# Kernel optimization log

Measured on AMD Instinct MI355X. Metric: run time of the kernel, lower is better.

Reference implementation:

```python
import jax, jax.numpy as jnp
import numpy as np
from math import sqrt

B, L, S, H, E = 4, 2048, 2048, 16, 64


def setup_inputs() -> dict:
    key = jax.random.key(0)
    kq, kk, kv = jax.random.split(key, 3)
    queries = jax.random.normal(kq, (B, L, H, E), dtype=jnp.float32)
    keys = jax.random.normal(kk, (B, S, H, E), dtype=jnp.float32)
    values = jax.random.normal(kv, (B, S, H, E), dtype=jnp.float32)
    # causal mask: True where attention is disallowed (upper triangle, excl diag)
    causal = jnp.triu(jnp.ones((L, S), dtype=jnp.bool_), k=1)
    attention_mask = jnp.broadcast_to(causal[None, None, :, :], (B, 1, L, S))
    return {"queries": queries, "keys": keys, "values": values,
            "attention_mask": attention_mask}


def reference(queries, keys, values, attention_mask):
    E_ = queries.shape[-1]
    scale = 1.0 / sqrt(E_)
    # [B,H,L,S] full score matrix (the quadratic intermediate of naive attention)
    scores = jnp.einsum('blhe,bshe->bhls', queries, keys)
    scores = jnp.where(attention_mask, -jnp.inf, scores)
    A = jnp.nan_to_num(jax.nn.softmax(scale * scores, axis=-1))
    V = jnp.einsum('bhls,bshd->blhd', A, values)
    return V
```

## Files before the change

kernel.cpp:

```cpp
#include <hip/hip_runtime.h>
#include <cmath>

#define B_ 4
#define L_ 2048
#define S_ 2048
#define H_ 16
#define E_ 64
#define SCALE2 0.18033688011112042f

typedef __attribute__((ext_vector_type(4))) float f32x4;
typedef __attribute__((ext_vector_type(8))) __bf16 bf16x8;
typedef __attribute__((ext_vector_type(8))) unsigned short ushort8;
union FragU { ushort8 u; bf16x8 b; unsigned int d[4]; };

__device__ __forceinline__ unsigned short f2bf(float f) {
    unsigned int u = __float_as_uint(f);
    return (unsigned short)((u + 0x7FFFu + ((u >> 16) & 1u)) >> 16);
}

__device__ __forceinline__ unsigned int pack_bf(float hi, float lo) {
    return __builtin_amdgcn_perm(__float_as_uint(hi), __float_as_uint(lo),
                                 0x07060302u);
}

__device__ __forceinline__ void gload_lds16(const void* g, void* l) {
    __builtin_amdgcn_global_load_lds(
        (const __attribute__((address_space(1))) void*)g,
        (__attribute__((address_space(3))) void*)l, 16, 0, 0);
}

__global__ __launch_bounds__(256) void conv_k(const float* __restrict__ K,
                                              unsigned short* __restrict__ Kbf) {
    const int idx = blockIdx.x * 256 + threadIdx.x;
    const int j   = idx & 7;
    const int row = idx >> 3;
    const int s   = row & (S_ - 1);
    const int bh  = row >> 11;
    const int h   = bh & (H_ - 1);
    const int b   = bh >> 4;
    const int jp  = j ^ (s & 7);
    const float* src = K + (((size_t)b * S_ + s) * H_ + h) * E_ + jp * 8;
    f32x4 a = *(const f32x4*)src;
    f32x4 d = *(const f32x4*)(src + 4);
    ushort8 u;
    u[0]=f2bf(a[0]); u[1]=f2bf(a[1]); u[2]=f2bf(a[2]); u[3]=f2bf(a[3]);
    u[4]=f2bf(d[0]); u[5]=f2bf(d[1]); u[6]=f2bf(d[2]); u[7]=f2bf(d[3]);
    *(ushort8*)(Kbf + (size_t)row * E_ + j * 8) = u;
}

__global__ __launch_bounds__(256) void conv_v(const float* __restrict__ V,
                                              unsigned short* __restrict__ Vt) {
    __shared__ unsigned short t[64 * 65];
    const int tid  = threadIdx.x;
    const int sblk = blockIdx.x & 31;
    const int h    = (blockIdx.x >> 5) & 15;
    const int b    = blockIdx.x >> 9;
    const int s0   = sblk * 64;
    for (int i = 0; i < 4; ++i) {
        const int c = tid + i * 256;
        const int sr = c >> 4, e0 = (c & 15) * 4;
        f32x4 a = *(const f32x4*)(V + (((size_t)b * S_ + s0 + sr) * H_ + h) * E_ + e0);
        t[sr * 65 + e0 + 0] = f2bf(a[0]);
        t[sr * 65 + e0 + 1] = f2bf(a[1]);
        t[sr * 65 + e0 + 2] = f2bf(a[2]);
        t[sr * 65 + e0 + 3] = f2bf(a[3]);
    }
    __syncthreads();
    for (int i = 0; i < 2; ++i) {
        const int c  = tid + i * 256;
        const int e  = c >> 3, cc = c & 7;
        const int q  = cc >> 1, half = cc & 1;
        ushort8 u;
        for (int j = 0; j < 8; ++j) {
            const int d = j >> 2, r = j & 3;
            const int key = (2 * half + d) * 16 + q * 4 + r;
            u[j] = t[key * 65 + e];
        }
        *(ushort8*)(Vt + ((size_t)(b * H_ + h) * E_ + e) * S_ + s0
                    + (cc ^ (e & 7)) * 8) = u;
    }
}

template <bool PRE>
__global__ __launch_bounds__(256, 4) void fattn_kernel(
    const float* __restrict__ Q, const unsigned short* __restrict__ Kbf,
    const unsigned short* __restrict__ Vt, const float* __restrict__ Kf,
    const float* __restrict__ Vf, float* __restrict__ Out)
{
    const int tid  = threadIdx.x;
    const int wave = tid >> 6;
    const int lane = tid & 63;
    const int ln   = lane & 15;
    const int quad = lane >> 4;
    const int qtile = gridDim.x - 1 - blockIdx.x;
    const int h = blockIdx.y;
    const int b = blockIdx.z;
    const int q0 = qtile * 64;
    const int qw = q0 + wave * 16;
    const int p7 = ln & 7;
    const int qrow = qw + ln;

    __shared__ __align__(16) unsigned short ldsK[64 * 64];
    __shared__ __align__(16) unsigned short ldsV[64 * 64];

    FragU qf[2];
    {
        const float* qp = Q + (((size_t)b * L_ + (qw + ln)) * H_ + h) * E_;
        for (int c = 0; c < 2; ++c) {
            const int e0 = c * 32 + quad * 8;
            f32x4 lo = *(const f32x4*)(qp + e0);
            f32x4 hi = *(const f32x4*)(qp + e0 + 4);
            ushort8 u;
            u[0]=f2bf(lo[0]*SCALE2); u[1]=f2bf(lo[1]*SCALE2);
            u[2]=f2bf(lo[2]*SCALE2); u[3]=f2bf(lo[3]*SCALE2);
            u[4]=f2bf(hi[0]*SCALE2); u[5]=f2bf(hi[1]*SCALE2);
            u[6]=f2bf(hi[2]*SCALE2); u[7]=f2bf(hi[3]*SCALE2);
            qf[c].u = u;
        }
    }

    f32x4 o[4];
    for (int et = 0; et < 4; ++et) o[et] = f32x4{0.f, 0.f, 0.f, 0.f};
    float lsum = 0.f;

    const unsigned short* kbh = Kbf + (size_t)(b * H_ + h) * S_ * E_;
    const unsigned short* vbh = Vt  + (size_t)(b * H_ + h) * E_ * S_;
    const float* kf32 = Kf + (((size_t)b * S_) * H_ + h) * E_;
    const float* vf32 = Vf + (((size_t)b * S_) * H_ + h) * E_;

    const int ntiles = qtile + 1;
    for (int kt = 0; kt < ntiles; ++kt) {
        const int k0 = kt * 64;
        __syncthreads();

        if constexpr (PRE) {
            const unsigned short* ktb = kbh + (size_t)k0 * E_;
            const unsigned short* vtb = vbh + k0;
            for (int i = 0; i < 2; ++i) {
                const int slot0 = wave * 128 + i * 64;
                gload_lds16(ktb + (size_t)(slot0 + lane) * 8, &ldsK[slot0 * 8]);
            }
            for (int i = 0; i < 2; ++i) {
                const int slot0 = wave * 128 + i * 64;
                const int slot  = slot0 + lane;
                const int e = slot >> 3, lc = slot & 7;
                gload_lds16(vtb + (size_t)e * S_ + lc * 8, &ldsV[slot0 * 8]);
            }
        } else {
            for (int i = 0; i < 2; ++i) {
                const int c = tid + i * 256;
                const int key = c >> 3, j = c & 7, jp = j ^ (key & 7);
                const float* src = kf32 + (size_t)(k0 + key) * (H_ * E_) + jp * 8;
                f32x4 a = *(const f32x4*)src, d = *(const f32x4*)(src + 4);
                ushort8 u;
                u[0]=f2bf(a[0]); u[1]=f2bf(a[1]); u[2]=f2bf(a[2]); u[3]=f2bf(a[3]);
                u[4]=f2bf(d[0]); u[5]=f2bf(d[1]); u[6]=f2bf(d[2]); u[7]=f2bf(d[3]);
                *(ushort8*)&ldsK[key * 64 + j * 8] = u;
            }
            for (int i = 0; i < 2; ++i) {
                const int c = tid + i * 256;
                const int e = c >> 3, cc = c & 7;
                const int q = cc >> 1, half = cc & 1;
                ushort8 u;
                for (int j = 0; j < 8; ++j) {
                    const int d = j >> 2, r = j & 3;
                    const int key = (2 * half + d) * 16 + q * 4 + r;
                    u[j] = f2bf(vf32[(size_t)(k0 + key) * (H_ * E_) + e]);
                }
                *(ushort8*)&ldsV[e * 64 + (cc ^ (e & 7)) * 8] = u;
            }
        }
        __syncthreads();

        f32x4 sfr[4];
        for (int n = 0; n < 4; ++n) {
            FragU kf0, kf1;
            kf0.u = *(const ushort8*)&ldsK[(n*16+ln)*64 + ((quad    ) ^ p7) * 8];
            kf1.u = *(const ushort8*)&ldsK[(n*16+ln)*64 + ((4 + quad) ^ p7) * 8];
            f32x4 acc = f32x4{0.f, 0.f, 0.f, 0.f};
            acc = __builtin_amdgcn_mfma_f32_16x16x32_bf16(kf0.b, qf[0].b, acc, 0, 0, 0);
            acc = __builtin_amdgcn_mfma_f32_16x16x32_bf16(kf1.b, qf[1].b, acc, 0, 0, 0);
            sfr[n] = acc;
        }

        const bool need_mask = (kt == qtile);
        unsigned int pk[4][2];
        for (int n = 0; n < 4; ++n) {
            float p[4];
            for (int r = 0; r < 4; ++r) {
                float v = __builtin_exp2f(sfr[n][r]);
                if (need_mask) {
                    const int key = k0 + n * 16 + quad * 4 + r;
                    v = (key <= qrow) ? v : 0.f;
                }
                lsum += v;
                p[r] = v;
            }
            pk[n][0] = pack_bf(p[1], p[0]);
            pk[n][1] = pack_bf(p[3], p[2]);
        }
        FragU pf0, pf1;
        pf0.d[0] = pk[0][0]; pf0.d[1] = pk[0][1];
        pf0.d[2] = pk[1][0]; pf0.d[3] = pk[1][1];
        pf1.d[0] = pk[2][0]; pf1.d[1] = pk[2][1];
        pf1.d[2] = pk[3][0]; pf1.d[3] = pk[3][1];

        for (int et = 0; et < 4; ++et) {
            FragU vf0, vf1;
            vf0.u = *(const ushort8*)&ldsV[(et*16+ln)*64 + ((2*quad    ) ^ p7) * 8];
            vf1.u = *(const ushort8*)&ldsV[(et*16+ln)*64 + ((2*quad + 1) ^ p7) * 8];
            o[et] = __builtin_amdgcn_mfma_f32_16x16x32_bf16(pf0.b, vf0.b, o[et], 0, 0, 0);
            o[et] = __builtin_amdgcn_mfma_f32_16x16x32_bf16(pf1.b, vf1.b, o[et], 0, 0, 0);
        }
    }

    lsum += __shfl_xor(lsum, 16);
    lsum += __shfl_xor(lsum, 32);
    const float inv = 1.f / lsum;

    for (int r = 0; r < 4; ++r) {
        const int row = quad * 4 + r;
        const float invr = __shfl(inv, row);
        float* op = Out + (((size_t)b * L_ + (qw + row)) * H_ + h) * E_;
        for (int et = 0; et < 4; ++et)
            op[et * 16 + ln] = o[et][r] * invr;
    }
}

extern "C" void kernel_launch(void* const* d_in, const int* in_sizes, int n_in,
                              void* d_out, int out_size, void* d_ws, size_t ws_size,
                              hipStream_t stream) {
    const float* Q = (const float*)d_in[0];
    const float* K = (const float*)d_in[1];
    const float* V = (const float*)d_in[2];
    float* Out = (float*)d_out;

    const size_t plane = (size_t)B_ * H_ * S_ * E_;
    unsigned short* Kbf = (unsigned short*)d_ws;
    unsigned short* Vt  = Kbf + plane;

    dim3 grid(L_ / 64, H_, B_);
    if (ws_size >= plane * 2 * sizeof(unsigned short)) {
        conv_k<<<(int)(plane / 8 / 256), 256, 0, stream>>>(K, Kbf);
        conv_v<<<B_ * H_ * (S_ / 64), 256, 0, stream>>>(V, Vt);
        fattn_kernel<true><<<grid, dim3(256), 0, stream>>>(Q, Kbf, Vt, K, V, Out);
    } else {
        fattn_kernel<false><<<grid, dim3(256), 0, stream>>>(Q, Kbf, Vt, K, V, Out);
    }
}
```

Before: 258.1 us.

## Enlarge query tile to 128 rows, double-buffer K/V LDS, stagger causal tile order

Result: faster. 250.6 us (-2.9%).

```diff
diff --git a/kernel.cpp b/kernel.cpp
--- a/kernel.cpp
+++ b/kernel.cpp
@@ -92,20 +92,21 @@
     const int lane = tid & 63;
     const int ln   = lane & 15;
     const int quad = lane >> 4;
-    const int qtile = gridDim.x - 1 - blockIdx.x;
+    const int qtile = (blockIdx.x + blockIdx.y + 4 * blockIdx.z) & 15;
     const int h = blockIdx.y;
     const int b = blockIdx.z;
-    const int q0 = qtile * 64;
-    const int qw = q0 + wave * 16;
+    const int q0 = qtile * 128;
+    const int qw = q0 + wave * 32;
     const int p7 = ln & 7;
-    const int qrow = qw + ln;
-
-    __shared__ __align__(16) unsigned short ldsK[64 * 64];
-    __shared__ __align__(16) unsigned short ldsV[64 * 64];
-
-    FragU qf[2];
-    {
-        const float* qp = Q + (((size_t)b * L_ + (qw + ln)) * H_ + h) * E_;
+
+    __shared__ __align__(16) unsigned short ldsK[2][64 * 64];
+    __shared__ __align__(16) unsigned short ldsV[2][64 * 64];
+
+    FragU qf[2][2];
+    #pragma unroll
+    for (int g = 0; g < 2; ++g) {
+        const float* qp = Q + (((size_t)b * L_ + (qw + g * 16 + ln)) * H_ + h) * E_;
+        #pragma unroll
         for (int c = 0; c < 2; ++c) {
             const int e0 = c * 32 + quad * 8;
             f32x4 lo = *(const f32x4*)(qp + e0);
@@ -115,115 +116,145 @@
             u[2]=f2bf(lo[2]*SCALE2); u[3]=f2bf(lo[3]*SCALE2);
             u[4]=f2bf(hi[0]*SCALE2); u[5]=f2bf(hi[1]*SCALE2);
             u[6]=f2bf(hi[2]*SCALE2); u[7]=f2bf(hi[3]*SCALE2);
-            qf[c].u = u;
-        }
-    }
-
-    f32x4 o[4];
-    for (int et = 0; et < 4; ++et) o[et] = f32x4{0.f, 0.f, 0.f, 0.f};
-    float lsum = 0.f;
+            qf[g][c].u = u;
+        }
+    }
+
+    f32x4 o[2][4];
+    #pragma unroll
+    for (int g = 0; g < 2; ++g)
+        #pragma unroll
+        for (int et = 0; et < 4; ++et) o[g][et] = f32x4{0.f, 0.f, 0.f, 0.f};
+    float lsum[2] = {0.f, 0.f};
 
     const unsigned short* kbh = Kbf + (size_t)(b * H_ + h) * S_ * E_;
     const unsigned short* vbh = Vt  + (size_t)(b * H_ + h) * E_ * S_;
     const float* kf32 = Kf + (((size_t)b * S_) * H_ + h) * E_;
     const float* vf32 = Vf + (((size_t)b * S_) * H_ + h) * E_;
 
-    const int ntiles = qtile + 1;
-    for (int kt = 0; kt < ntiles; ++kt) {
-        const int k0 = kt * 64;
-        __syncthreads();
-
+    auto STAGE = [&](int bsel, int kt2) {
+        const int k0s = kt2 * 64;
         if constexpr (PRE) {
-            const unsigned short* ktb = kbh + (size_t)k0 * E_;
-            const unsigned short* vtb = vbh + k0;
+            const unsigned short* ktb = kbh + (size_t)k0s * E_;
+            const unsigned short* vtb = vbh + k0s;
+            #pragma unroll
             for (int i = 0; i < 2; ++i) {
                 const int slot0 = wave * 128 + i * 64;
-                gload_lds16(ktb + (size_t)(slot0 + lane) * 8, &ldsK[slot0 * 8]);
-            }
+                gload_lds16(ktb + (size_t)(slot0 + lane) * 8,
+                            &ldsK[bsel][slot0 * 8]);
+            }
+            #pragma unroll
             for (int i = 0; i < 2; ++i) {
                 const int slot0 = wave * 128 + i * 64;
                 const int slot  = slot0 + lane;
                 const int e = slot >> 3, lc = slot & 7;
-                gload_lds16(vtb + (size_t)e * S_ + lc * 8, &ldsV[slot0 * 8]);
+                gload_lds16(vtb + (size_t)e * S_ + lc * 8,
+                            &ldsV[bsel][slot0 * 8]);
             }
         } else {
+            #pragma unroll
             for (int i = 0; i < 2; ++i) {
                 const int c = tid + i * 256;
                 const int key = c >> 3, j = c & 7, jp = j ^ (key & 7);
-                const float* src = kf32 + (size_t)(k0 + key) * (H_ * E_) + jp * 8;
+                const float* src = kf32 + (size_t)(k0s + key) * (H_ * E_) + jp * 8;
                 f32x4 a = *(const f32x4*)src, d = *(const f32x4*)(src + 4);
                 ushort8 u;
                 u[0]=f2bf(a[0]); u[1]=f2bf(a[1]); u[2]=f2bf(a[2]); u[3]=f2bf(a[3]);
                 u[4]=f2bf(d[0]); u[5]=f2bf(d[1]); u[6]=f2bf(d[2]); u[7]=f2bf(d[3]);
-                *(ushort8*)&ldsK[key * 64 + j * 8] = u;
-            }
+                *(ushort8*)&ldsK[bsel][key * 64 + j * 8] = u;
+            }
+            #pragma unroll
             for (int i = 0; i < 2; ++i) {
                 const int c = tid + i * 256;
                 const int e = c >> 3, cc = c & 7;
                 const int q = cc >> 1, half = cc & 1;
                 ushort8 u;
+                #pragma unroll
                 for (int j = 0; j < 8; ++j) {
                     const int d = j >> 2, r = j & 3;
                     const int key = (2 * half + d) * 16 + q * 4 + r;
-                    u[j] = f2bf(vf32[(size_t)(k0 + key) * (H_ * E_) + e]);
+                    u[j] = f2bf(vf32[(size_t)(k0s + key) * (H_ * E_) + e]);
                 }
-                *(ushort8*)&ldsV[e * 64 + (cc ^ (e & 7)) * 8] = u;
-            }
-        }
+                *(ushort8*)&ldsV[bsel][e * 64 + (cc ^ (e & 7)) * 8] = u;
+            }
+        }
+    };
+
+    const int ntiles = 2 * qtile + 2;
+    STAGE(0, 0);
+    int cur = 0;
+    for (int kt = 0; kt < ntiles; ++kt) {
+        const int k0 = kt * 64;
         __syncthreads();
-
-        f32x4 sfr[4];
-        for (int n = 0; n < 4; ++n) {
-            FragU kf0, kf1;
-            kf0.u = *(const ushort8*)&ldsK[(n*16+ln)*64 + ((quad    ) ^ p7) * 8];
-            kf1.u = *(const ushort8*)&ldsK[(n*16+ln)*64 + ((4 + quad) ^ p7) * 8];
-            f32x4 acc = f32x4{0.f, 0.f, 0.f, 0.f};
-            acc = __builtin_amdgcn_mfma_f32_16x16x32_bf16(kf0.b, qf[0].b, acc, 0, 0, 0);
-            acc = __builtin_amdgcn_mfma_f32_16x16x32_bf16(kf1.b, qf[1].b, acc, 0, 0, 0);
-            sfr[n] = acc;
-        }
-
-        const bool need_mask = (kt == qtile);
-        unsigned int pk[4][2];
-        for (int n = 0; n < 4; ++n) {
-            float p[4];
-            for (int r = 0; r < 4; ++r) {
-                float v = __builtin_exp2f(sfr[n][r]);
-                if (need_mask) {
-                    const int key = k0 + n * 16 + quad * 4 + r;
-                    v = (key <= qrow) ? v : 0.f;
+        if (kt + 1 < ntiles) STAGE(cur ^ 1, kt + 1);
+
+        if (k0 <= qw + 31) {
+            __builtin_amdgcn_s_setprio(1);
+            const unsigned short* bK = ldsK[cur];
+            const unsigned short* bV = ldsV[cur];
+            const bool m0 = (k0 + 63 > qw);
+            const bool m1 = (k0 + 63 > qw + 16);
+
+            FragU pf[2][2];
+            #pragma unroll
+            for (int n = 0; n < 4; ++n) {
+                FragU kf0, kf1;
+                kf0.u = *(const ushort8*)&bK[(n*16+ln)*64 + ((quad    ) ^ p7) * 8];
+                kf1.u = *(const ushort8*)&bK[(n*16+ln)*64 + ((4 + quad) ^ p7) * 8];
+                #pragma unroll
+                for (int g = 0; g < 2; ++g) {
+                    f32x4 acc = f32x4{0.f, 0.f, 0.f, 0.f};
+                    acc = __builtin_amdgcn_mfma_f32_16x16x32_bf16(kf0.b, qf[g][0].b, acc, 0, 0, 0);
+                    acc = __builtin_amdgcn_mfma_f32_16x16x32_bf16(kf1.b, qf[g][1].b, acc, 0, 0, 0);
+                    const bool nm = g ? m1 : m0;
+                    const int qrow = qw + g * 16 + ln;
+                    float p[4];
+                    #pragma unroll
+                    for (int r = 0; r < 4; ++r) {
+                        float v = __builtin_exp2f(acc[r]);
+                        if (nm) {
+                            const int key = k0 + n * 16 + quad * 4 + r;
+                            v = (key <= qrow) ? v : 0.f;
+                        }
+                        p[r] = v;
+                    }
+                    lsum[g] += (p[0] + p[1]) + (p[2] + p[3]);
+                    pf[g][n >> 1].d[(n & 1) * 2 + 0] = pack_bf(p[1], p[0]);
+                    pf[g][n >> 1].d[(n & 1) * 2 + 1] = pack_bf(p[3], p[2]);
                 }
-                lsum += v;
-                p[r] = v;
-            }
-            pk[n][0] = pack_bf(p[1], p[0]);
-            pk[n][1] = pack_bf(p[3], p[2]);
-        }
-        FragU pf0, pf1;
-        pf0.d[0] = pk[0][0]; pf0.d[1] = pk[0][1];
-        pf0.d[2] = pk[1][0]; pf0.d[3] = pk[1][1];
-        pf1.d[0] = pk[2][0]; pf1.d[1] = pk[2][1];
-        pf1.d[2] = pk[3][0]; pf1.d[3] = pk[3][1];
-
-        for (int et = 0; et < 4; ++et) {
-            FragU vf0, vf1;
-            vf0.u = *(const ushort8*)&ldsV[(et*16+ln)*64 + ((2*quad    ) ^ p7) * 8];
-            vf1.u = *(const ushort8*)&ldsV[(et*16+ln)*64 + ((2*quad + 1) ^ p7) * 8];
-            o[et] = __builtin_amdgcn_mfma_f32_16x16x32_bf16(pf0.b, vf0.b, o[et], 0, 0, 0);
-            o[et] = __builtin_amdgcn_mfma_f32_16x16x32_bf16(pf1.b, vf1.b, o[et], 0, 0, 0);
-        }
-    }
-
-    lsum += __shfl_xor(lsum, 16);
-    lsum += __shfl_xor(lsum, 32);
-    const float inv = 1.f / lsum;
-
-    for (int r = 0; r < 4; ++r) {
-        const int row = quad * 4 + r;
-        const float invr = __shfl(inv, row);
-        float* op = Out + (((size_t)b * L_ + (qw + row)) * H_ + h) * E_;
-        for (int et = 0; et < 4; ++et)
-            op[et * 16 + ln] = o[et][r] * invr;
+            }
+
+            #pragma unroll
+            for (int et = 0; et < 4; ++et) {
+                FragU vf0, vf1;
+                vf0.u = *(const ushort8*)&bV[(et*16+ln)*64 + ((2*quad    ) ^ p7) * 8];
+                vf1.u = *(const ushort8*)&bV[(et*16+ln)*64 + ((2*quad + 1) ^ p7) * 8];
+                #pragma unroll
+                for (int g = 0; g < 2; ++g) {
+                    o[g][et] = __builtin_amdgcn_mfma_f32_16x16x32_bf16(pf[g][0].b, vf0.b, o[g][et], 0, 0, 0);
+                    o[g][et] = __builtin_amdgcn_mfma_f32_16x16x32_bf16(pf[g][1].b, vf1.b, o[g][et], 0, 0, 0);
+                }
+            }
+            __builtin_amdgcn_s_setprio(0);
+        }
+        cur ^= 1;
+    }
+
+    #pragma unroll
+    for (int g = 0; g < 2; ++g) {
+        float l = lsum[g];
+        l += __shfl_xor(l, 16);
+        l += __shfl_xor(l, 32);
+        const float inv = 1.f / l;
+        #pragma unroll
+        for (int r = 0; r < 4; ++r) {
+            const int row = quad * 4 + r;
+            const float invr = __shfl(inv, row);
+            float* op = Out + (((size_t)b * L_ + (qw + g * 16 + row)) * H_ + h) * E_;
+            #pragma unroll
+            for (int et = 0; et < 4; ++et)
+                op[et * 16 + ln] = o[g][et][r] * invr;
+        }
     }
 }
 
@@ -239,7 +270,7 @@
     unsigned short* Kbf = (unsigned short*)d_ws;
     unsigned short* Vt  = Kbf + plane;
 
-    dim3 grid(L_ / 64, H_, B_);
+    dim3 grid(L_ / 128, H_, B_);
     if (ws_size >= plane * 2 * sizeof(unsigned short)) {
         conv_k<<<(int)(plane / 8 / 256), 256, 0, stream>>>(K, Kbf);
         conv_v<<<B_ * H_ * (S_ / 64), 256, 0, stream>>>(V, Vt);
```
